# Kernel optimization log

Hardware: AMD Instinct MI355X
Metric: run time of the kernel (lower is better)

## Reference

```python
import jax, jax.numpy as jnp
import numpy as np

B, L, EMB, OUT, H = 32, 1024, 512, 64, 8


def setup_inputs() -> dict:
    key = jax.random.key(0)
    ks = jax.random.split(key, 9)
    joint = jax.random.normal(ks[0], (B, L, EMB), dtype=jnp.float32)
    delta = jax.random.normal(ks[1], (B, L, L, 2), dtype=jnp.float32)
    traj_len = jax.random.randint(ks[2], (B,), 0, L, dtype=jnp.int64)
    s = 1.0 / np.sqrt(EMB)
    Wq = jax.random.uniform(ks[3], (H, EMB, OUT), dtype=jnp.float32, minval=-s, maxval=s)
    Wk = jax.random.uniform(ks[4], (H, EMB, OUT), dtype=jnp.float32, minval=-s, maxval=s)
    Wv = jax.random.uniform(ks[5], (H, EMB, OUT), dtype=jnp.float32, minval=-s, maxval=s)
    bq = jax.random.uniform(ks[6], (H, OUT), dtype=jnp.float32, minval=-s, maxval=s)
    bk = jax.random.uniform(ks[7], (H, OUT), dtype=jnp.float32, minval=-s, maxval=s)
    bv = jax.random.uniform(ks[8], (H, OUT), dtype=jnp.float32, minval=-s, maxval=s)
    so = 1.0 / np.sqrt(H * OUT)
    Wo = jax.random.uniform(jax.random.fold_in(key, 99), (H * OUT, OUT), dtype=jnp.float32, minval=-so, maxval=so)
    return {"joint": joint, "delta": delta, "traj_len": traj_len,
            "Wq": Wq, "Wk": Wk, "Wv": Wv, "bq": bq, "bk": bk, "bv": bv, "Wo": Wo}


def reference(joint, delta, traj_len, Wq, Wk, Wv, bq, bk, bv, Wo):
    # delta is reduced only to define the mask shape [B, L, L]
    _ = jnp.sum(delta, -1)
    idx = jnp.arange(L)
    valid = idx[None, :] < traj_len[:, None]            # [B, L]
    mask = (valid[:, :, None] & valid[:, None, :]).astype(jnp.float32)  # [B, L, L]

    # per-head QKV, vectorized over heads
    q = jnp.einsum('ble,heo->bhlo', joint, Wq) + bq[None, :, None, :]
    k = jnp.einsum('ble,heo->bhlo', joint, Wk) + bk[None, :, None, :]
    v = jnp.einsum('ble,heo->bhlo', joint, Wv) + bv[None, :, None, :]

    scale = 1.0 / jnp.sqrt(jnp.float32(joint.shape[-1]))
    attn = jnp.einsum('bhqo,bhko->bhqk', q, k) * scale
    attn = attn * mask[:, None, :, :]                   # multiplicative mask (faithful)
    attn = jax.nn.softmax(attn, axis=-1)
    out = jnp.einsum('bhqk,bhko->bhqo', attn, v)        # [B, H, L, OUT]
    concat = out.transpose(0, 2, 1, 3).reshape(B, L, H * OUT)
    return concat @ Wo                                  # [B, L, OUT]
```

## Files before the change

kernel.cpp:

```cpp
#include <hip/hip_runtime.h>
#include <math.h>

#define BB 32
#define LL 1024
#define EMB 512
#define DOUT 64
#define NH 8

typedef __attribute__((ext_vector_type(8))) short short8;
typedef __attribute__((ext_vector_type(4))) short short4v;
typedef __attribute__((ext_vector_type(8))) _Float16 half8;
typedef __attribute__((ext_vector_type(4))) float f32x4;

union S8 { short8 v; unsigned u[4]; };

__device__ __forceinline__ unsigned pk2(float a, float b) {
    unsigned ua = __float_as_uint(a);
    ua += 0x7fffu + ((ua >> 16) & 1u);
    unsigned ub = __float_as_uint(b);
    ub += 0x7fffu + ((ub >> 16) & 1u);
    return (ua >> 16) | (ub & 0xffff0000u);
}
__device__ __forceinline__ unsigned short pk1(float a) {
    unsigned ua = __float_as_uint(a);
    ua += 0x7fffu + ((ua >> 16) & 1u);
    return (unsigned short)(ua >> 16);
}
__device__ __forceinline__ float bf2f(unsigned short u) {
    return __uint_as_float(((unsigned)u) << 16);
}

__global__ __launch_bounds__(256) void convert_kernel(
    const float* __restrict__ joint,
    const float* __restrict__ Wq, const float* __restrict__ Wk, const float* __restrict__ Wv,
    const float* __restrict__ Wo,
    _Float16* __restrict__ Xh, _Float16* __restrict__ Wth,
    unsigned short* __restrict__ Wotb)
{
    const int blk = blockIdx.x;
    const int tid = threadIdx.x;
    if (blk < 8192) {
        const size_t idx = ((size_t)blk * 256 + tid) * 8;
        const float4 a = *reinterpret_cast<const float4*>(&joint[idx]);
        const float4 b = *reinterpret_cast<const float4*>(&joint[idx + 4]);
        half8 h;
        h[0] = (_Float16)a.x; h[1] = (_Float16)a.y; h[2] = (_Float16)a.z; h[3] = (_Float16)a.w;
        h[4] = (_Float16)b.x; h[5] = (_Float16)b.y; h[6] = (_Float16)b.z; h[7] = (_Float16)b.w;
        *reinterpret_cast<half8*>(&Xh[idx]) = h;
    } else if (blk < 8192 + 384) {
        const int gid = (blk - 8192) * 256 + tid;
        const int y = gid >> 12;
        const int rem = gid & 4095;
        const int n = rem >> 6;
        const int k8 = rem & 63;
        const int h = y / 3, mat = y - 3 * h;
        const float* W = (mat == 0 ? Wq : (mat == 1 ? Wk : Wv)) + (size_t)h * EMB * DOUT;
        half8 t;
        #pragma unroll
        for (int i = 0; i < 8; ++i)
            t[i] = (_Float16)W[(size_t)(k8 * 8 + i) * DOUT + n];
        *reinterpret_cast<half8*>(&Wth[(size_t)y * 32768 + n * 512 + k8 * 8]) = t;
    } else {
        const int gid = (blk - 8576) * 256 + tid;
        const int n = gid >> 6;
        const int k8 = gid & 63;
        short4v lo, hi;
        #pragma unroll
        for (int i = 0; i < 4; ++i) lo[i] = (short)pk1(Wo[(size_t)(k8 * 8 + i) * DOUT + n]);
        #pragma unroll
        for (int i = 0; i < 4; ++i) hi[i] = (short)pk1(Wo[(size_t)(k8 * 8 + 4 + i) * DOUT + n]);
        *reinterpret_cast<short4v*>(&Wotb[(size_t)n * 512 + k8 * 8]) = lo;
        *reinterpret_cast<short4v*>(&Wotb[(size_t)n * 512 + k8 * 8 + 4]) = hi;
    }
}

template <bool VMODE>
__device__ __forceinline__ void qkv_core(
    const _Float16* __restrict__ Xh, const _Float16* __restrict__ Wy,
    _Float16* As, _Float16* Bs, f32x4 (&acc)[8], int rowbase)
{
    const int tid = threadIdx.x;
    const int lane = tid & 63;
    const int wid = tid >> 6;
    const int lq = lane & 15;
    const int quad = lane >> 4;

    for (int kb = 0; kb < EMB; kb += 64) {
        __syncthreads();
        #pragma unroll
        for (int p = 0; p < 4; ++p) {
            const int bidx = tid + p * 256;
            const int m = bidx >> 3, j = bidx & 7;
            const half8 t = *reinterpret_cast<const half8*>(
                &Xh[(size_t)(rowbase + m) * EMB + kb + 8 * j]);
            *reinterpret_cast<half8*>(&As[m * 64 + 8 * (j ^ (m & 7))]) = t;
        }
        #pragma unroll
        for (int p = 0; p < 2; ++p) {
            const int bidx = tid + p * 256;
            const int n = bidx >> 3, j = bidx & 7;
            const half8 t = *reinterpret_cast<const half8*>(
                &Wy[(size_t)n * EMB + kb + 8 * j]);
            *reinterpret_cast<half8*>(&Bs[n * 64 + 8 * (j ^ (n & 7))]) = t;
        }
        __syncthreads();

        half8 xf[2][2], wf[4][2];
        #pragma unroll
        for (int mt = 0; mt < 2; ++mt)
            #pragma unroll
            for (int kf = 0; kf < 2; ++kf) {
                const int row = wid * 32 + mt * 16 + lq;
                xf[mt][kf] = *reinterpret_cast<const half8*>(
                    &As[row * 64 + 8 * ((4 * kf + quad) ^ (row & 7))]);
            }
        #pragma unroll
        for (int nt = 0; nt < 4; ++nt)
            #pragma unroll
            for (int kf = 0; kf < 2; ++kf)
                wf[nt][kf] = *reinterpret_cast<const half8*>(
                    &Bs[(nt * 16 + lq) * 64 + 8 * ((4 * kf + quad) ^ (lq & 7))]);

        #pragma unroll
        for (int mt = 0; mt < 2; ++mt)
            #pragma unroll
            for (int nt = 0; nt < 4; ++nt)
                #pragma unroll
                for (int kf = 0; kf < 2; ++kf) {
                    if (VMODE)
                        acc[mt * 4 + nt] = __builtin_amdgcn_mfma_f32_16x16x32_f16(
                            xf[mt][kf], wf[nt][kf], acc[mt * 4 + nt], 0, 0, 0);
                    else
                        acc[mt * 4 + nt] = __builtin_amdgcn_mfma_f32_16x16x32_f16(
                            wf[nt][kf], xf[mt][kf], acc[mt * 4 + nt], 0, 0, 0);
                }
    }
}

__global__ __launch_bounds__(256) void qkv_mfma(
    const _Float16* __restrict__ Xh, const _Float16* __restrict__ Wth,
    const float* __restrict__ bq, const float* __restrict__ bk, const float* __restrict__ bv,
    unsigned short* __restrict__ Qb, unsigned short* __restrict__ Kb,
    unsigned short* __restrict__ Vb)
{
    __shared__ __align__(16) _Float16 As[128 * 64];
    __shared__ __align__(16) _Float16 Bs[64 * 64];

    const int tid = threadIdx.x;
    const int lane = tid & 63;
    const int wid = tid >> 6;
    const int lq = lane & 15;
    const int quad = lane >> 4;

    const int rowbase = blockIdx.x * 128;
    const int y = blockIdx.y;
    const int mat = y % 3;
    const int h = y / 3;
    const _Float16* Wy = Wth + (size_t)y * 32768;
    const float* bias = (mat == 0 ? bq : (mat == 1 ? bk : bv)) + (size_t)h * DOUT;
    unsigned short* Out = (mat == 0 ? Qb : (mat == 1 ? Kb : Vb));

    f32x4 acc[8];
    #pragma unroll
    for (int i = 0; i < 8; ++i) { acc[i][0] = 0.f; acc[i][1] = 0.f; acc[i][2] = 0.f; acc[i][3] = 0.f; }

    const int b_ = rowbase >> 10;
    const int lb = rowbase & 1023;
    const size_t baseh = ((size_t)b_ * NH + h);

    if (mat == 2) {
        qkv_core<true>(Xh, Wy, As, Bs, acc, rowbase);
        #pragma unroll
        for (int nt = 0; nt < 4; ++nt) {
            const int d = nt * 16 + lq;
            const float bz = bias[d];
            #pragma unroll
            for (int mt = 0; mt < 2; ++mt) {
                short4v s;
                #pragma unroll
                for (int r = 0; r < 4; ++r) s[r] = (short)pk1(acc[mt * 4 + nt][r] + bz);
                *reinterpret_cast<short4v*>(
                    &Out[(baseh * DOUT + d) * LL + lb + wid * 32 + mt * 16 + quad * 4]) = s;
            }
        }
    } else {
        qkv_core<false>(Xh, Wy, As, Bs, acc, rowbase);
        #pragma unroll
        for (int nt = 0; nt < 4; ++nt) {
            const float4 bz = *reinterpret_cast<const float4*>(&bias[nt * 16 + quad * 4]);
            const float bzv[4] = {bz.x, bz.y, bz.z, bz.w};
            #pragma unroll
            for (int mt = 0; mt < 2; ++mt) {
                const int l = lb + wid * 32 + mt * 16 + lq;
                short4v s;
                #pragma unroll
                for (int r = 0; r < 4; ++r) s[r] = (short)pk1(acc[mt * 4 + nt][r] + bzv[r]);
                *reinterpret_cast<short4v*>(
                    &Out[(baseh * LL + l) * DOUT + nt * 16 + quad * 4]) = s;
            }
        }
    }
}

__global__ __launch_bounds__(64) void vsuf_kernel(
    const unsigned short* __restrict__ Vb, const int* __restrict__ traj_len,
    float* __restrict__ Vsuf)
{
    const int bh = blockIdx.x;
    const int b = bh >> 3;
    const int d = threadIdx.x;
    int len = traj_len[b];
    if (len < 0) len = 0;
    if (len > LL) len = LL;

    const unsigned short* src = Vb + ((size_t)bh * DOUT + d) * LL;
    float s = 0.f;
    int l = len;
    for (; l < LL && (l & 7); ++l) s += bf2f(src[l]);
    for (; l < LL; l += 8) {
        const short8 v = *reinterpret_cast<const short8*>(&src[l]);
        #pragma unroll
        for (int i = 0; i < 8; ++i) s += bf2f((unsigned short)v[i]);
    }
    Vsuf[bh * DOUT + d] = s;
}

__global__ __launch_bounds__(256, 3) void attn_kernel(
    const unsigned short* __restrict__ Qb,
    const unsigned short* __restrict__ Kb,
    const unsigned short* __restrict__ Vb,
    const float* __restrict__ Vsuf,
    const int* __restrict__ traj_len,
    unsigned short* __restrict__ Ob)
{
    __shared__ __align__(16) short lds[16384];
    short* Ks = lds;
    short* Vt = lds + 4096;

    const int tid = threadIdx.x;
    const int lane = tid & 63;
    const int wid = tid >> 6;
    const int lq = lane & 15;
    const int quad = lane >> 4;
    short* Ps = lds + 8192 + wid * 2048;

    const int qt = blockIdx.x;
    const int h = blockIdx.y;
    const int b = blockIdx.z;

    int len = traj_len[b];
    if (len < 0) len = 0;
    if (len > LL) len = LL;

    const size_t base = ((size_t)b * NH + h) * LL * DOUT;
    const int qbase = qt * 128 + wid * 32;

    short8 qf[2][2];
    #pragma unroll
    for (int g = 0; g < 2; ++g)
        #pragma unroll
        for (int kf = 0; kf < 2; ++kf)
            qf[g][kf] = *reinterpret_cast<const short8*>(
                &Qb[base + (size_t)(qbase + 16 * g + lq) * DOUT + kf * 32 + quad * 8]);

    const float SC = 0.04419417382415922f;
    float Mq[2];
    Mq[0] = ((qbase + lq) < len) ? SC : 0.0f;
    Mq[1] = ((qbase + 16 + lq) < len) ? SC : 0.0f;
    const int krel = len - 4 * quad;

    f32x4 o[2][4];
    #pragma unroll
    for (int g = 0; g < 2; ++g)
        #pragma unroll
        for (int nt = 0; nt < 4; ++nt) {
            o[g][nt][0] = 0.f; o[g][nt][1] = 0.f; o[g][nt][2] = 0.f; o[g][nt][3] = 0.f;
        }
    float l_acc[2] = {0.0f, 0.0f};

    const int kend = ((len + 63) >> 6) << 6;

    for (int kt = 0; kt < kend; kt += 64) {
        __syncthreads();
        #pragma unroll
        for (int p = 0; p < 2; ++p) {
            const int bidx = tid + p * 256;
            const int m = bidx >> 3, j = bidx & 7;
            const short8 tk = *reinterpret_cast<const short8*>(
                &Kb[base + (size_t)(kt + m) * DOUT + 8 * j]);
            *reinterpret_cast<short8*>(&Ks[m * 64 + 8 * (j ^ (m & 7))]) = tk;
            const short8 tv = *reinterpret_cast<const short8*>(
                &Vb[base + (size_t)m * LL + kt + 8 * j]);
            *reinterpret_cast<short8*>(&Vt[m * 64 + 8 * (j ^ (m & 7))]) = tv;
        }
        __syncthreads();

        f32x4 sS[2][4];
        #pragma unroll
        for (int nt = 0; nt < 4; ++nt) {
            const int krow = (16 * nt + lq) * 64;
            const short8 k0 = *reinterpret_cast<const short8*>(&Ks[krow + 8 * ((0 + quad) ^ (lq & 7))]);
            const short8 k1 = *reinterpret_cast<const short8*>(&Ks[krow + 8 * ((4 + quad) ^ (lq & 7))]);
            #pragma unroll
            for (int g = 0; g < 2; ++g) {
                f32x4 z;
                z[0] = 0.f; z[1] = 0.f; z[2] = 0.f; z[3] = 0.f;
                z = __builtin_amdgcn_mfma_f32_16x16x32_bf16(k0, qf[g][0], z, 0, 0, 0);
                z = __builtin_amdgcn_mfma_f32_16x16x32_bf16(k1, qf[g][1], z, 0, 0, 0);
                sS[g][nt] = z;
            }
        }

        #pragma unroll
        for (int g = 0; g < 2; ++g) {
            #pragma unroll
            for (int nt = 0; nt < 4; ++nt) {
                float pv[4];
                #pragma unroll
                for (int r = 0; r < 4; ++r) {
                    const bool kv = (kt + 16 * nt + r) < krel;
                    pv[r] = kv ? __expf(sS[g][nt][r] * Mq[g]) : 0.0f;
                    l_acc[g] += pv[r];
                }
                int2 w;
                w.x = (int)pk2(pv[0], pv[1]);
                w.y = (int)pk2(pv[2], pv[3]);
                *reinterpret_cast<int2*>(
                    &Ps[(16 * g + lq) * 64 + 8 * ((2 * nt + (quad >> 1)) ^ (lq & 7)) + 4 * (quad & 1)]) = w;
            }
        }

        short8 pf[2][2];
        #pragma unroll
        for (int g = 0; g < 2; ++g)
            #pragma unroll
            for (int kf = 0; kf < 2; ++kf)
                pf[g][kf] = *reinterpret_cast<const short8*>(
                    &Ps[(16 * g + lq) * 64 + 8 * ((4 * kf + quad) ^ (lq & 7))]);

        #pragma unroll
        for (int nt = 0; nt < 4; ++nt) {
            const int vrow = (16 * nt + lq) * 64;
            const short8 v0 = *reinterpret_cast<const short8*>(&Vt[vrow + 8 * ((0 + quad) ^ (lq & 7))]);
            const short8 v1 = *reinterpret_cast<const short8*>(&Vt[vrow + 8 * ((4 + quad) ^ (lq & 7))]);
            #pragma unroll
            for (int g = 0; g < 2; ++g) {
                o[g][nt] = __builtin_amdgcn_mfma_f32_16x16x32_bf16(pf[g][0], v0, o[g][nt], 0, 0, 0);
                o[g][nt] = __builtin_amdgcn_mfma_f32_16x16x32_bf16(pf[g][1], v1, o[g][nt], 0, 0, 0);
            }
        }
    }

    const float lext = (float)(LL - len);
    float inv[2];
    #pragma unroll
    for (int g = 0; g < 2; ++g) {
        float t = l_acc[g];
        t += __shfl_xor(t, 16);
        t += __shfl_xor(t, 32);
        inv[g] = 1.0f / (t + lext);
    }
    float iq[2][4];
    #pragma unroll
    for (int g = 0; g < 2; ++g)
        #pragma unroll
        for (int r = 0; r < 4; ++r)
            iq[g][r] = __shfl(inv[g], 4 * quad + r, 64);

    const float* vsufp = &Vsuf[((size_t)b * NH + h) * DOUT];
    #pragma unroll
    for (int g = 0; g < 2; ++g) {
        #pragma unroll
        for (int nt = 0; nt < 4; ++nt) {
            const float vs = vsufp[16 * nt + lq];
            #pragma unroll
            for (int r = 0; r < 4; ++r) {
                const int qrow = qbase + 16 * g + 4 * quad + r;
                const float val = (o[g][nt][r] + vs) * iq[g][r];
                Ob[((size_t)b * LL + qrow) * 512 + h * 64 + 16 * nt + lq] = pk1(val);
            }
        }
    }
}

__global__ __launch_bounds__(256) void outproj_mfma(
    const unsigned short* __restrict__ Ob,
    const unsigned short* __restrict__ Wotb,
    float* __restrict__ out)
{
    __shared__ __align__(16) short As[128 * 64];
    __shared__ __align__(16) short Bs[64 * 64];

    const int tid = threadIdx.x;
    const int lane = tid & 63;
    const int wid = tid >> 6;
    const int lq = lane & 15;
    const int quad = lane >> 4;
    const int rowbase = blockIdx.x * 128;

    f32x4 acc[8];
    #pragma unroll
    for (int i = 0; i < 8; ++i) { acc[i][0] = 0.f; acc[i][1] = 0.f; acc[i][2] = 0.f; acc[i][3] = 0.f; }

    for (int kb = 0; kb < 512; kb += 64) {
        __syncthreads();
        #pragma unroll
        for (int p = 0; p < 4; ++p) {
            const int bidx = tid + p * 256;
            const int m = bidx >> 3, j = bidx & 7;
            const short8 t = *reinterpret_cast<const short8*>(
                &Ob[(size_t)(rowbase + m) * 512 + kb + 8 * j]);
            *reinterpret_cast<short8*>(&As[m * 64 + 8 * (j ^ (m & 7))]) = t;
        }
        #pragma unroll
        for (int p = 0; p < 2; ++p) {
            const int bidx = tid + p * 256;
            const int n = bidx >> 3, j = bidx & 7;
            const short8 t = *reinterpret_cast<const short8*>(
                &Wotb[(size_t)n * 512 + kb + 8 * j]);
            *reinterpret_cast<short8*>(&Bs[n * 64 + 8 * (j ^ (n & 7))]) = t;
        }
        __syncthreads();

        short8 xf[2][2], wf[4][2];
        #pragma unroll
        for (int mt = 0; mt < 2; ++mt)
            #pragma unroll
            for (int kf = 0; kf < 2; ++kf) {
                const int row = wid * 32 + mt * 16 + lq;
                xf[mt][kf] = *reinterpret_cast<const short8*>(
                    &As[row * 64 + 8 * ((4 * kf + quad) ^ (row & 7))]);
            }
        #pragma unroll
        for (int nt = 0; nt < 4; ++nt)
            #pragma unroll
            for (int kf = 0; kf < 2; ++kf)
                wf[nt][kf] = *reinterpret_cast<const short8*>(
                    &Bs[(nt * 16 + lq) * 64 + 8 * ((4 * kf + quad) ^ (lq & 7))]);

        #pragma unroll
        for (int mt = 0; mt < 2; ++mt)
            #pragma unroll
            for (int nt = 0; nt < 4; ++nt)
                #pragma unroll
                for (int kf = 0; kf < 2; ++kf)
                    acc[mt * 4 + nt] = __builtin_amdgcn_mfma_f32_16x16x32_bf16(
                        wf[nt][kf], xf[mt][kf], acc[mt * 4 + nt], 0, 0, 0);
    }

    #pragma unroll
    for (int nt = 0; nt < 4; ++nt)
        #pragma unroll
        for (int mt = 0; mt < 2; ++mt) {
            const int row = rowbase + wid * 32 + mt * 16 + lq;
            float4 ov;
            ov.x = acc[mt * 4 + nt][0];
            ov.y = acc[mt * 4 + nt][1];
            ov.z = acc[mt * 4 + nt][2];
            ov.w = acc[mt * 4 + nt][3];
            *reinterpret_cast<float4*>(&out[(size_t)row * DOUT + nt * 16 + quad * 4]) = ov;
        }
}

extern "C" void kernel_launch(void* const* d_in, const int* in_sizes, int n_in,
                              void* d_out, int out_size, void* d_ws, size_t ws_size,
                              hipStream_t stream) {
    const float* joint = (const float*)d_in[0];
    const int* traj = (const int*)d_in[2];
    const float* Wq = (const float*)d_in[3];
    const float* Wk = (const float*)d_in[4];
    const float* Wv = (const float*)d_in[5];
    const float* bq = (const float*)d_in[6];
    const float* bk = (const float*)d_in[7];
    const float* bv = (const float*)d_in[8];
    const float* Wo = (const float*)d_in[9];
    float* out = (float*)d_out;

    char* ws = (char*)d_ws;
    _Float16* Xh          = (_Float16*)(ws);
    _Float16* Wth         = (_Float16*)(ws + 33554432);
    unsigned short* Wotb  = (unsigned short*)(ws + 35127296);
    unsigned short* Qb    = (unsigned short*)(ws + 35192832);
    unsigned short* Kb    = (unsigned short*)(ws + 68747264);
    unsigned short* Vb    = (unsigned short*)(ws + 102301696);
    unsigned short* Ob    = (unsigned short*)(ws + 135856128);
    float* Vsuf           = (float*)(ws + 169410560);

    convert_kernel<<<8592, 256, 0, stream>>>(joint, Wq, Wk, Wv, Wo, Xh, Wth, Wotb);
    qkv_mfma<<<dim3(256, 24), 256, 0, stream>>>(Xh, Wth, bq, bk, bv, Qb, Kb, Vb);
    vsuf_kernel<<<256, 64, 0, stream>>>(Vb, traj, Vsuf);
    attn_kernel<<<dim3(8, NH, BB), 256, 0, stream>>>(Qb, Kb, Vb, Vsuf, traj, Ob);
    outproj_mfma<<<256, 256, 0, stream>>>(Ob, Wotb, out);
}
```

Baseline: 559.3 us.

## Use direct global-to-LDS loads in GEMMs and parallelize V suffix sum

The QKV and output-projection GEMM tile loads now use global_load_lds, writing straight into shared memory with the XOR swizzle moved to the source address. This avoids the round trip through registers. The V suffix-sum kernel now uses 256 threads per block, with lanes striding across the sequence and a shuffle reduction, replacing one serial thread per column. It relies on the per-wave contiguous LDS destination matching the swizzled layout, and it adds an explicit vmcnt drain before each barrier.

```diff
diff --git a/kernel.cpp b/kernel.cpp
--- a/kernel.cpp
+++ b/kernel.cpp
@@ -11,8 +11,6 @@
 typedef __attribute__((ext_vector_type(4))) short short4v;
 typedef __attribute__((ext_vector_type(8))) _Float16 half8;
 typedef __attribute__((ext_vector_type(4))) float f32x4;
-
-union S8 { short8 v; unsigned u[4]; };
 
 __device__ __forceinline__ unsigned pk2(float a, float b) {
     unsigned ua = __float_as_uint(a);
@@ -28,6 +26,17 @@
 }
 __device__ __forceinline__ float bf2f(unsigned short u) {
     return __uint_as_float(((unsigned)u) << 16);
+}
+
+__device__ __forceinline__ void gload16(const void* g, void* l) {
+    __builtin_amdgcn_global_load_lds(
+        (const __attribute__((address_space(1))) void*)g,
+        (__attribute__((address_space(3))) void*)l,
+        16, 0, 0);
+}
+
+__device__ __forceinline__ void drain_vmcnt() {
+    asm volatile("s_waitcnt vmcnt(0)" ::: "memory");
 }
 
 __global__ __launch_bounds__(256) void convert_kernel(
@@ -91,18 +100,19 @@
         for (int p = 0; p < 4; ++p) {
             const int bidx = tid + p * 256;
             const int m = bidx >> 3, j = bidx & 7;
-            const half8 t = *reinterpret_cast<const half8*>(
-                &Xh[(size_t)(rowbase + m) * EMB + kb + 8 * j]);
-            *reinterpret_cast<half8*>(&As[m * 64 + 8 * (j ^ (m & 7))]) = t;
+            const int jx = j ^ (m & 7);
+            gload16(&Xh[(size_t)(rowbase + m) * EMB + kb + 8 * jx],
+                    &As[(p * 256 + wid * 64) * 8]);
         }
         #pragma unroll
         for (int p = 0; p < 2; ++p) {
             const int bidx = tid + p * 256;
             const int n = bidx >> 3, j = bidx & 7;
-            const half8 t = *reinterpret_cast<const half8*>(
-                &Wy[(size_t)n * EMB + kb + 8 * j]);
-            *reinterpret_cast<half8*>(&Bs[n * 64 + 8 * (j ^ (n & 7))]) = t;
-        }
+            const int jx = j ^ (n & 7);
+            gload16(&Wy[(size_t)n * EMB + kb + 8 * jx],
+                    &Bs[(p * 256 + wid * 64) * 8]);
+        }
+        drain_vmcnt();
         __syncthreads();
 
         half8 xf[2][2], wf[4][2];
@@ -202,27 +212,43 @@
     }
 }
 
-__global__ __launch_bounds__(64) void vsuf_kernel(
+__global__ __launch_bounds__(256) void vsuf_kernel(
     const unsigned short* __restrict__ Vb, const int* __restrict__ traj_len,
     float* __restrict__ Vsuf)
 {
     const int bh = blockIdx.x;
     const int b = bh >> 3;
-    const int d = threadIdx.x;
+    const int tid = threadIdx.x;
+    const int lane = tid & 63;
+    const int wid = tid >> 6;
     int len = traj_len[b];
     if (len < 0) len = 0;
     if (len > LL) len = LL;
-
-    const unsigned short* src = Vb + ((size_t)bh * DOUT + d) * LL;
-    float s = 0.f;
-    int l = len;
-    for (; l < LL && (l & 7); ++l) s += bf2f(src[l]);
-    for (; l < LL; l += 8) {
-        const short8 v = *reinterpret_cast<const short8*>(&src[l]);
-        #pragma unroll
-        for (int i = 0; i < 8; ++i) s += bf2f((unsigned short)v[i]);
-    }
-    Vsuf[bh * DOUT + d] = s;
+    const int l0 = len & ~7;
+
+    #pragma unroll
+    for (int i = 0; i < 16; ++i) {
+        const int d = wid * 16 + i;
+        const unsigned short* src = Vb + ((size_t)bh * DOUT + d) * LL;
+        float s = 0.f;
+        #pragma unroll
+        for (int p = 0; p < 2; ++p) {
+            const int l = l0 + p * 512 + lane * 8;
+            if (l < LL) {
+                const short8 v = *reinterpret_cast<const short8*>(&src[l]);
+                #pragma unroll
+                for (int q = 0; q < 8; ++q)
+                    if (l + q >= len) s += bf2f((unsigned short)v[q]);
+            }
+        }
+        s += __shfl_xor(s, 1);
+        s += __shfl_xor(s, 2);
+        s += __shfl_xor(s, 4);
+        s += __shfl_xor(s, 8);
+        s += __shfl_xor(s, 16);
+        s += __shfl_xor(s, 32);
+        if (lane == 0) Vsuf[(size_t)bh * DOUT + d] = s;
+    }
 }
 
 __global__ __launch_bounds__(256, 3) void attn_kernel(
@@ -408,18 +434,19 @@
         for (int p = 0; p < 4; ++p) {
             const int bidx = tid + p * 256;
             const int m = bidx >> 3, j = bidx & 7;
-            const short8 t = *reinterpret_cast<const short8*>(
-                &Ob[(size_t)(rowbase + m) * 512 + kb + 8 * j]);
-            *reinterpret_cast<short8*>(&As[m * 64 + 8 * (j ^ (m & 7))]) = t;
+            const int jx = j ^ (m & 7);
+            gload16(&Ob[(size_t)(rowbase + m) * 512 + kb + 8 * jx],
+                    &As[(p * 256 + wid * 64) * 8]);
         }
         #pragma unroll
         for (int p = 0; p < 2; ++p) {
             const int bidx = tid + p * 256;
             const int n = bidx >> 3, j = bidx & 7;
-            const short8 t = *reinterpret_cast<const short8*>(
-                &Wotb[(size_t)n * 512 + kb + 8 * j]);
-            *reinterpret_cast<short8*>(&Bs[n * 64 + 8 * (j ^ (n & 7))]) = t;
-        }
+            const int jx = j ^ (n & 7);
+            gload16(&Wotb[(size_t)n * 512 + kb + 8 * jx],
+                    &Bs[(p * 256 + wid * 64) * 8]);
+        }
+        drain_vmcnt();
         __syncthreads();
 
         short8 xf[2][2], wf[4][2];
@@ -488,7 +515,7 @@
 
     convert_kernel<<<8592, 256, 0, stream>>>(joint, Wq, Wk, Wv, Wo, Xh, Wth, Wotb);
     qkv_mfma<<<dim3(256, 24), 256, 0, stream>>>(Xh, Wth, bq, bk, bv, Qb, Kb, Vb);
-    vsuf_kernel<<<256, 64, 0, stream>>>(Vb, traj, Vsuf);
+    vsuf_kernel<<<256, 256, 0, stream>>>(Vb, traj, Vsuf);
     attn_kernel<<<dim3(8, NH, BB), 256, 0, stream>>>(Qb, Kb, Vb, Vsuf, traj, Ob);
     outproj_mfma<<<256, 256, 0, stream>>>(Ob, Wotb, out);
 }
```

Result: faster. 523.8 us (-6.3%).
